# Performance work log

Hardware: AMD Instinct MI355X
Metric: run time of the kernel (lower is better)

The kernel has to match this reference:

```python
import jax, jax.numpy as jnp
import numpy as np

B, S, H, FFN, E = 2, 2048, 1024, 4096, 8

def setup_inputs() -> dict:
    key = jax.random.key(0)
    k0, k1, k2, k3 = jax.random.split(key, 4)
    return {
        "hidden_states": jax.random.normal(k0, (B, S, H), dtype=jnp.float32),
        "Wr": jax.random.normal(k1, (H, E), dtype=jnp.float32) * 0.02,
        "br": jnp.zeros((E,), dtype=jnp.float32),
        "W1": jax.random.normal(k2, (E, H, FFN), dtype=jnp.float32) * 0.02,
        "W2": jax.random.normal(k3, (E, FFN, H), dtype=jnp.float32) * 0.02,
    }

def reference(hidden_states, Wr, br, W1, W2):
    b, s, h = hidden_states.shape
    x = hidden_states.reshape(-1, h)                      # [T, H]
    # sinkhorn routing branch in forward: sigmoid activation then top-1
    route = jax.nn.sigmoid(x @ Wr + br)                   # [T, E]
    max_prob = jnp.max(route, axis=1, keepdims=True)      # [T, 1]
    max_ind = jnp.argmax(route, axis=1)                   # [T] int
    out = jnp.zeros_like(x)
    n_experts = Wr.shape[1]
    for e in range(n_experts):  # small fixed expert set
        mask = (max_ind == e)[:, None].astype(x.dtype)    # [T, 1] dispatch mask
        # expert MLP: fc2(gelu(fc1(x))), no bias (add_bias_linear=False)
        y = jax.nn.gelu(x @ W1[e], approximate=False) @ W2[e]  # [T, H]
        out = out + mask * y                              # scatter-combine
    out = out * max_prob                                  # scale by router prob
    return out.reshape(b, s, h)
```

## Files before the change

kernel.cpp:

```cpp
#include <hip/hip_runtime.h>
#include <hip/hip_bf16.h>
#include <math.h>

#define TOK 4096
#define HD 1024
#define FD 4096
#define NE 8
#define MBLK 8

typedef __attribute__((ext_vector_type(4))) float f32x4;
typedef __attribute__((ext_vector_type(8))) short s16x8;
typedef __attribute__((ext_vector_type(4))) unsigned int u32x4;

typedef const __attribute__((address_space(1))) void g_void;
typedef __attribute__((address_space(3))) void lds_void;

__device__ __forceinline__ unsigned short f2bf(float f) {
    union { float f; unsigned u; } v; v.f = f;
    unsigned r = v.u + 0x7FFFu + ((v.u >> 16) & 1u);
    return (unsigned short)(r >> 16);
}

__device__ __forceinline__ unsigned cvt2(float a, float b) {
    unsigned r;
    asm("v_cvt_pk_bf16_f32 %0, %1, %2" : "=v"(r) : "v"(a), "v"(b));
    return r;
}

__global__ void router_kernel(const float* __restrict__ x, const float* __restrict__ Wr,
                              const float* __restrict__ br, int* __restrict__ counts,
                              int* __restrict__ tlist, float* __restrict__ mprob,
                              unsigned short* __restrict__ xb) {
    const int lane = threadIdx.x & 63;
    const int t = blockIdx.x * 4 + (threadIdx.x >> 6);
    const float* xr = x + (size_t)t * HD;
    unsigned short* xbr = xb + (size_t)t * HD;
    float acc[NE];
#pragma unroll
    for (int e = 0; e < NE; ++e) acc[e] = 0.f;
    for (int h = lane; h < HD; h += 64) {
        float xv = xr[h];
        xbr[h] = f2bf(xv);
        f32x4 w0 = *(const f32x4*)(Wr + h * NE);
        f32x4 w1 = *(const f32x4*)(Wr + h * NE + 4);
        acc[0] += xv * w0.x; acc[1] += xv * w0.y; acc[2] += xv * w0.z; acc[3] += xv * w0.w;
        acc[4] += xv * w1.x; acc[5] += xv * w1.y; acc[6] += xv * w1.z; acc[7] += xv * w1.w;
    }
#pragma unroll
    for (int off = 32; off >= 1; off >>= 1)
#pragma unroll
        for (int e = 0; e < NE; ++e) acc[e] += __shfl_down(acc[e], off, 64);
    if (lane == 0) {
        float best = -1.f; int bi = 0;
#pragma unroll
        for (int e = 0; e < NE; ++e) {
            float r = 1.f / (1.f + expf(-(acc[e] + br[e])));
            if (r > best) { best = r; bi = e; }
        }
        mprob[t] = best;
        int pos = atomicAdd(&counts[bi], 1);
        tlist[bi * TOK + pos] = t;
    }
}

template<int K, int N>
__global__ __launch_bounds__(256)
void transpose_cast(const float* __restrict__ src, unsigned short* __restrict__ dst) {
    __shared__ unsigned short T[128 * 64];
    const int e  = blockIdx.z;
    const int n0 = blockIdx.x * 128;
    const int k0 = blockIdx.y * 64;
    const int tid = threadIdx.x;
    {
        const int gg = tid & 7;
        const int cg = tid >> 3;
        const float* sp = src + ((size_t)e * K + k0 + gg * 8) * N + n0 + (cg << 2);
        f32x4 v[8];
#pragma unroll
        for (int j = 0; j < 8; ++j) v[j] = *(const f32x4*)(sp + (size_t)j * N);
#pragma unroll
        for (int i = 0; i < 4; ++i) {
            int n = (cg << 2) + i;
            u32x4 q;
            q.x = cvt2(v[0][i], v[1][i]);
            q.y = cvt2(v[2][i], v[3][i]);
            q.z = cvt2(v[4][i], v[5][i]);
            q.w = cvt2(v[6][i], v[7][i]);
            *(u32x4*)&T[(n << 6) + (((gg + n) & 7) << 3)] = q;
        }
    }
    __syncthreads();
    {
        const int n = tid >> 1;
        const int half = tid & 1;
        unsigned short* op = dst + ((size_t)e * N + n0 + n) * K + k0 + half * 32;
#pragma unroll
        for (int j = 0; j < 4; ++j) {
            int kg = half * 4 + j;
            s16x8 c = *(const s16x8*)&T[(n << 6) + (((kg + n) & 7) << 3)];
            *(s16x8*)(op + j * 8) = c;
        }
    }
}

template<int K, bool FC1, int KSPLIT>
__global__ __launch_bounds__(256, 2)
void expert_gemm(const unsigned short* __restrict__ Asrc, const unsigned short* __restrict__ Wt,
                 const int* __restrict__ counts, const int* __restrict__ tlist,
                 const float* __restrict__ mprob,
                 unsigned short* __restrict__ inter, float* __restrict__ out) {
    constexpr int NDIM = FC1 ? FD : HD;
    constexpr int KC = K / KSPLIT;
    constexpr int NT = KC / 64;
    const int e  = (KSPLIT == 1) ? (int)blockIdx.y : ((int)blockIdx.y & (NE - 1));
    const int ks = (KSPLIT == 1) ? 0 : ((int)blockIdx.y >> 3);
    const int kbase = ks * KC;
    const int cnt = counts[e];
    const int m0 = blockIdx.z * 128;
    if (m0 >= cnt) return;
    const int n0 = blockIdx.x * 128;

    __shared__ unsigned short Al[2][128 * 64];
    __shared__ unsigned short Bl[2][128 * 64];

    const int tid = threadIdx.x;
    const int lane = tid & 63;
    const int wave = tid >> 6;

    const unsigned short* aptr[4];
    const unsigned short* bptr[4];
    {
        int lr = lane >> 3, g = lane & 7;
#pragma unroll
        for (int it = 0; it < 4; ++it) {
            int r = wave * 32 + it * 8 + lr;
            int kg = (g - r) & 7;
            int m = m0 + r;
            int tk = (m < cnt) ? tlist[e * TOK + m] : 0;
            aptr[it] = Asrc + (size_t)tk * K + kbase + kg * 8;
            bptr[it] = Wt + ((size_t)e * NDIM + n0 + r) * K + kbase + kg * 8;
        }
    }

    const int wrow = (wave >> 1) << 6;
    const int wcol = (wave & 1) << 6;
    const int lm = lane & 15, quad = lane >> 4;

    f32x4 acc[4][4] = {};

#pragma unroll
    for (int it = 0; it < 4; ++it) {
        __builtin_amdgcn_global_load_lds((g_void*)aptr[it],
            (lds_void*)&Al[0][wave * 2048 + it * 512], 16, 0, 0);
        __builtin_amdgcn_global_load_lds((g_void*)bptr[it],
            (lds_void*)&Bl[0][wave * 2048 + it * 512], 16, 0, 0);
        aptr[it] += 64; bptr[it] += 64;
    }

    for (int t = 0; t < NT; ++t) {
        const int buf = t & 1;
        asm volatile("s_waitcnt vmcnt(0)" ::: "memory");
        __builtin_amdgcn_s_barrier();
        if (t + 1 < NT) {
#pragma unroll
            for (int it = 0; it < 4; ++it) {
                __builtin_amdgcn_global_load_lds((g_void*)aptr[it],
                    (lds_void*)&Al[buf ^ 1][wave * 2048 + it * 512], 16, 0, 0);
                __builtin_amdgcn_global_load_lds((g_void*)bptr[it],
                    (lds_void*)&Bl[buf ^ 1][wave * 2048 + it * 512], 16, 0, 0);
                aptr[it] += 64; bptr[it] += 64;
            }
            __builtin_amdgcn_sched_barrier(0);
        }
        const unsigned short* Ab = &Al[buf][0];
        const unsigned short* Bb = &Bl[buf][0];
#pragma unroll
        for (int kt = 0; kt < 2; ++kt) {
            s16x8 af[4], bf[4];
            int gk = (kt << 2) + quad;
#pragma unroll
            for (int mt = 0; mt < 4; ++mt) {
                int m = wrow + (mt << 4) + lm;
                af[mt] = *(const s16x8*)&Ab[(m << 6) + (((gk + m) & 7) << 3)];
            }
#pragma unroll
            for (int nt = 0; nt < 4; ++nt) {
                int n = wcol + (nt << 4) + lm;
                bf[nt] = *(const s16x8*)&Bb[(n << 6) + (((gk + n) & 7) << 3)];
            }
#pragma unroll
            for (int mt = 0; mt < 4; ++mt)
#pragma unroll
                for (int nt = 0; nt < 4; ++nt)
                    acc[mt][nt] = __builtin_amdgcn_mfma_f32_16x16x32_bf16(
                        af[mt], bf[nt], acc[mt][nt], 0, 0, 0);
        }
    }

#pragma unroll
    for (int mt = 0; mt < 4; ++mt) {
#pragma unroll
        for (int r = 0; r < 4; ++r) {
            int row = wrow + (mt << 4) + (quad << 2) + r;
            if (m0 + row >= cnt) continue;
            int tk = tlist[e * TOK + m0 + row];
            int colb = n0 + wcol + lm;
            if constexpr (FC1) {
#pragma unroll
                for (int nt = 0; nt < 4; ++nt) {
                    float v = acc[mt][nt][r];
                    float g = 0.5f * v * (1.f + erff(v * 0.70710678f));
                    inter[(size_t)tk * FD + colb + (nt << 4)] = f2bf(g);
                }
            } else {
                float p = mprob[tk];
#pragma unroll
                for (int nt = 0; nt < 4; ++nt)
                    atomicAdd(&out[(size_t)tk * HD + colb + (nt << 4)], acc[mt][nt][r] * p);
            }
        }
    }
}

extern "C" void kernel_launch(void* const* d_in, const int* in_sizes, int n_in,
                              void* d_out, int out_size, void* d_ws, size_t ws_size,
                              hipStream_t stream) {
    const float* x  = (const float*)d_in[0];
    const float* Wr = (const float*)d_in[1];
    const float* br = (const float*)d_in[2];
    const float* W1 = (const float*)d_in[3];
    const float* W2 = (const float*)d_in[4];
    float* out = (float*)d_out;

    char* ws = (char*)d_ws;
    int* counts           = (int*)ws;
    float* mprob          = (float*)(ws + 256);
    int* tlist            = (int*)(ws + 16640);
    unsigned short* xb    = (unsigned short*)(ws + 147712);
    unsigned short* inter = (unsigned short*)(ws + 8536320);
    unsigned short* Wt    = (unsigned short*)(ws + 42090752);

    hipMemsetAsync(counts, 0, NE * sizeof(int), stream);
    hipMemsetAsync(out, 0, (size_t)out_size * sizeof(float), stream);
    router_kernel<<<TOK / 4, 256, 0, stream>>>(x, Wr, br, counts, tlist, mprob, xb);

    transpose_cast<HD, FD><<<dim3(FD / 128, HD / 64, NE), 256, 0, stream>>>(W1, Wt);
    expert_gemm<HD, true, 1><<<dim3(FD / 128, NE, MBLK), 256, 0, stream>>>(
        xb, Wt, counts, tlist, mprob, inter, nullptr);

    transpose_cast<FD, HD><<<dim3(HD / 128, FD / 64, NE), 256, 0, stream>>>(W2, Wt);
    expert_gemm<FD, false, 2><<<dim3(HD / 128, NE * 2, MBLK), 256, 0, stream>>>(
        inter, Wt, counts, tlist, mprob, nullptr, out);
}
```

Before: 555.8 us.

## Halve GEMM K-tile with a shared A/B LDS buffer and rework the transpose-cast kernel

The expert GEMM now stages a 32-wide K slice per step, packing A and B into one shared LDS buffer with an interleaved swizzle. This halves LDS use per block, and launch bounds are raised to allow 4 blocks per CU instead of 2. The transpose_cast kernel is also rewritten: it stages packed bf16 pairs in a 32-bit LDS tile and each thread gathers 16 words before issuing its vector stores. The smaller K step doubles the barrier and wait count per unit of work in exchange for more occupancy, and the higher block count may force register spills.

```diff
diff --git a/kernel.cpp b/kernel.cpp
--- a/kernel.cpp
+++ b/kernel.cpp
@@ -66,52 +66,51 @@
 template<int K, int N>
 __global__ __launch_bounds__(256)
 void transpose_cast(const float* __restrict__ src, unsigned short* __restrict__ dst) {
-    __shared__ unsigned short T[128 * 64];
+    __shared__ unsigned int T32[32 * 128];
     const int e  = blockIdx.z;
     const int n0 = blockIdx.x * 128;
     const int k0 = blockIdx.y * 64;
     const int tid = threadIdx.x;
     {
-        const int gg = tid & 7;
-        const int cg = tid >> 3;
-        const float* sp = src + ((size_t)e * K + k0 + gg * 8) * N + n0 + (cg << 2);
-        f32x4 v[8];
-#pragma unroll
-        for (int j = 0; j < 8; ++j) v[j] = *(const f32x4*)(sp + (size_t)j * N);
-#pragma unroll
-        for (int i = 0; i < 4; ++i) {
-            int n = (cg << 2) + i;
+        const int kp0 = tid >> 5;
+        const int c4  = (tid & 31) << 2;
+        const float* sp = src + ((size_t)e * K + k0 + kp0 * 2) * N + n0 + c4;
+#pragma unroll
+        for (int it = 0; it < 4; ++it) {
+            f32x4 r0 = *(const f32x4*)sp;
+            f32x4 r1 = *(const f32x4*)(sp + N);
             u32x4 q;
-            q.x = cvt2(v[0][i], v[1][i]);
-            q.y = cvt2(v[2][i], v[3][i]);
-            q.z = cvt2(v[4][i], v[5][i]);
-            q.w = cvt2(v[6][i], v[7][i]);
-            *(u32x4*)&T[(n << 6) + (((gg + n) & 7) << 3)] = q;
+            q.x = cvt2(r0.x, r1.x);
+            q.y = cvt2(r0.y, r1.y);
+            q.z = cvt2(r0.z, r1.z);
+            q.w = cvt2(r0.w, r1.w);
+            *(u32x4*)&T32[(it * 8 + kp0) * 128 + c4] = q;
+            sp += (size_t)16 * N;
         }
     }
     __syncthreads();
     {
-        const int n = tid >> 1;
-        const int half = tid & 1;
+        const int n = tid >> 1, half = tid & 1;
+        unsigned int r[16];
+#pragma unroll
+        for (int j = 0; j < 16; ++j) r[j] = T32[(half * 16 + j) * 128 + n];
         unsigned short* op = dst + ((size_t)e * N + n0 + n) * K + k0 + half * 32;
-#pragma unroll
-        for (int j = 0; j < 4; ++j) {
-            int kg = half * 4 + j;
-            s16x8 c = *(const s16x8*)&T[(n << 6) + (((kg + n) & 7) << 3)];
-            *(s16x8*)(op + j * 8) = c;
-        }
+        *(u32x4*)(op)      = *(const u32x4*)&r[0];
+        *(u32x4*)(op + 8)  = *(const u32x4*)&r[4];
+        *(u32x4*)(op + 16) = *(const u32x4*)&r[8];
+        *(u32x4*)(op + 24) = *(const u32x4*)&r[12];
     }
 }
 
 template<int K, bool FC1, int KSPLIT>
-__global__ __launch_bounds__(256, 2)
+__global__ __launch_bounds__(256, 4)
 void expert_gemm(const unsigned short* __restrict__ Asrc, const unsigned short* __restrict__ Wt,
                  const int* __restrict__ counts, const int* __restrict__ tlist,
                  const float* __restrict__ mprob,
                  unsigned short* __restrict__ inter, float* __restrict__ out) {
     constexpr int NDIM = FC1 ? FD : HD;
     constexpr int KC = K / KSPLIT;
-    constexpr int NT = KC / 64;
+    constexpr int NT = KC / 32;
     const int e  = (KSPLIT == 1) ? (int)blockIdx.y : ((int)blockIdx.y & (NE - 1));
     const int ks = (KSPLIT == 1) ? 0 : ((int)blockIdx.y >> 3);
     const int kbase = ks * KC;
@@ -120,25 +119,23 @@
     if (m0 >= cnt) return;
     const int n0 = blockIdx.x * 128;
 
-    __shared__ unsigned short Al[2][128 * 64];
-    __shared__ unsigned short Bl[2][128 * 64];
+    __shared__ unsigned short L[2][128 * 64];
 
     const int tid = threadIdx.x;
     const int lane = tid & 63;
     const int wave = tid >> 6;
 
-    const unsigned short* aptr[4];
-    const unsigned short* bptr[4];
-    {
-        int lr = lane >> 3, g = lane & 7;
-#pragma unroll
-        for (int it = 0; it < 4; ++it) {
-            int r = wave * 32 + it * 8 + lr;
-            int kg = (g - r) & 7;
+    const unsigned short* gp[4];
+#pragma unroll
+    for (int i = 0; i < 4; ++i) {
+        int r = i * 32 + wave * 8 + (lane >> 3);
+        int diff = ((lane & 7) - r) & 7;
+        if (diff < 4) {
             int m = m0 + r;
             int tk = (m < cnt) ? tlist[e * TOK + m] : 0;
-            aptr[it] = Asrc + (size_t)tk * K + kbase + kg * 8;
-            bptr[it] = Wt + ((size_t)e * NDIM + n0 + r) * K + kbase + kg * 8;
+            gp[i] = Asrc + (size_t)tk * K + kbase + diff * 8;
+        } else {
+            gp[i] = Wt + ((size_t)e * NDIM + n0 + r) * K + kbase + (diff - 4) * 8;
         }
     }
 
@@ -149,12 +146,10 @@
     f32x4 acc[4][4] = {};
 
 #pragma unroll
-    for (int it = 0; it < 4; ++it) {
-        __builtin_amdgcn_global_load_lds((g_void*)aptr[it],
-            (lds_void*)&Al[0][wave * 2048 + it * 512], 16, 0, 0);
-        __builtin_amdgcn_global_load_lds((g_void*)bptr[it],
-            (lds_void*)&Bl[0][wave * 2048 + it * 512], 16, 0, 0);
-        aptr[it] += 64; bptr[it] += 64;
+    for (int i = 0; i < 4; ++i) {
+        __builtin_amdgcn_global_load_lds((g_void*)gp[i],
+            (lds_void*)&L[0][i * 2048 + wave * 512], 16, 0, 0);
+        gp[i] += 32;
     }
 
     for (int t = 0; t < NT; ++t) {
@@ -163,38 +158,31 @@
         __builtin_amdgcn_s_barrier();
         if (t + 1 < NT) {
 #pragma unroll
-            for (int it = 0; it < 4; ++it) {
-                __builtin_amdgcn_global_load_lds((g_void*)aptr[it],
-                    (lds_void*)&Al[buf ^ 1][wave * 2048 + it * 512], 16, 0, 0);
-                __builtin_amdgcn_global_load_lds((g_void*)bptr[it],
-                    (lds_void*)&Bl[buf ^ 1][wave * 2048 + it * 512], 16, 0, 0);
-                aptr[it] += 64; bptr[it] += 64;
+            for (int i = 0; i < 4; ++i) {
+                __builtin_amdgcn_global_load_lds((g_void*)gp[i],
+                    (lds_void*)&L[buf ^ 1][i * 2048 + wave * 512], 16, 0, 0);
+                gp[i] += 32;
             }
             __builtin_amdgcn_sched_barrier(0);
         }
-        const unsigned short* Ab = &Al[buf][0];
-        const unsigned short* Bb = &Bl[buf][0];
-#pragma unroll
-        for (int kt = 0; kt < 2; ++kt) {
-            s16x8 af[4], bf[4];
-            int gk = (kt << 2) + quad;
-#pragma unroll
-            for (int mt = 0; mt < 4; ++mt) {
-                int m = wrow + (mt << 4) + lm;
-                af[mt] = *(const s16x8*)&Ab[(m << 6) + (((gk + m) & 7) << 3)];
-            }
-#pragma unroll
-            for (int nt = 0; nt < 4; ++nt) {
-                int n = wcol + (nt << 4) + lm;
-                bf[nt] = *(const s16x8*)&Bb[(n << 6) + (((gk + n) & 7) << 3)];
-            }
-#pragma unroll
-            for (int mt = 0; mt < 4; ++mt)
-#pragma unroll
-                for (int nt = 0; nt < 4; ++nt)
-                    acc[mt][nt] = __builtin_amdgcn_mfma_f32_16x16x32_bf16(
-                        af[mt], bf[nt], acc[mt][nt], 0, 0, 0);
-        }
+        const unsigned short* Lb = &L[buf][0];
+        s16x8 af[4], bf[4];
+#pragma unroll
+        for (int mt = 0; mt < 4; ++mt) {
+            int m = wrow + (mt << 4) + lm;
+            af[mt] = *(const s16x8*)&Lb[(m << 6) + (((quad + m) & 7) << 3)];
+        }
+#pragma unroll
+        for (int nt = 0; nt < 4; ++nt) {
+            int n = wcol + (nt << 4) + lm;
+            bf[nt] = *(const s16x8*)&Lb[(n << 6) + (((4 + quad + n) & 7) << 3)];
+        }
+#pragma unroll
+        for (int mt = 0; mt < 4; ++mt)
+#pragma unroll
+            for (int nt = 0; nt < 4; ++nt)
+                acc[mt][nt] = __builtin_amdgcn_mfma_f32_16x16x32_bf16(
+                    af[mt], bf[nt], acc[mt][nt], 0, 0, 0);
     }
 
 #pragma unroll
```

Measured after the change: 519.4 us. 6.5% less time.
